# Kernel tuning notes

Hardware: AMD Instinct MI355X
Metric: run time of the kernel (lower is better)

The kernel has to match this reference:

```python
import jax, jax.numpy as jnp
import numpy as np

# Config constants (match init_kwargs)
N_EXPERTS = 8
CAPACITY = 1280
W_IMPORTANCE = 0.01
W_LOAD = 0.01
LAMBDA_Z = 0.001
W_PENALTY = 0.01


def setup_inputs() -> dict:
    key = jax.random.key(0)
    ks = jax.random.split(key, 6)
    B, T, C, E, F = 4, 2048, 1024, N_EXPERTS, 4096
    s = 0.02
    return {
        "x": jax.random.normal(ks[0], (B, T, C), dtype=jnp.float32),
        "gate_w": jax.random.normal(ks[1], (E, C), dtype=jnp.float32) * s,
        "gate_b": jnp.zeros((E,), dtype=jnp.float32),
        "w1": jax.random.normal(ks[2], (E, F, C), dtype=jnp.float32) * s,
        "b1": jnp.zeros((E, F), dtype=jnp.float32),
        "w2": jax.random.normal(ks[3], (E, C, F), dtype=jnp.float32) * s,
        "b2": jnp.zeros((E, C), dtype=jnp.float32),
    }


def reference(x, gate_w, gate_b, w1, b1, w2, b2):
    B, T, C = x.shape
    E = N_EXPERTS
    xf = x.reshape(B * T, C)
    bt = xf.shape[0]

    # ---- routing ----
    gate_logits = xf @ gate_w.T + gate_b  # (BT, E)

    # penalty loss
    p = jax.nn.softmax(gate_logits / 1.66, axis=-1)
    pen_a = jnp.mean(p * (1.0 - p))
    pm = p.mean(axis=0)
    pen_b = 1.0 / E - jnp.mean(pm * (1.0 - pm))
    penalty = W_PENALTY * (pen_a + pen_b)

    # z-loss
    z_loss = LAMBDA_Z * jnp.mean(jax.nn.logsumexp(gate_logits, axis=-1) ** 2)

    router_probs = jax.nn.softmax(gate_logits.astype(jnp.float32), axis=-1).astype(x.dtype)
    top1_idx = jnp.argmax(router_probs, axis=-1)        # (BT,)
    top1_w = jnp.max(router_probs, axis=-1)             # (BT,)
    onehot = jax.nn.one_hot(top1_idx, E, dtype=jnp.int32)

    # capacity masking: position of each token within its chosen expert
    priority = jnp.cumsum(onehot, axis=0)               # (BT, E)
    pos = priority[jnp.arange(bt), top1_idx] - 1        # (BT,)
    keep = pos < CAPACITY                               # (BT,) bool

    # load-balance loss
    f_i = onehot.astype(x.dtype).mean(axis=0)
    P_i = router_probs.mean(axis=0)
    load_loss = W_LOAD * E * jnp.sum(f_i * P_i)

    # importance loss (scatter of top1 probs == onehot-weighted sum)
    importance = (onehot.astype(x.dtype) * top1_w[:, None]).sum(axis=0)  # (E,)
    cv2 = jnp.var(importance) / jnp.mean(importance) ** 2
    importance_loss = W_IMPORTANCE * cv2

    aux_loss = penalty + z_loss + load_loss + importance_loss

    # ---- dispatch -> grouped FFN -> combine ----
    pos_c = jnp.clip(pos, 0, CAPACITY - 1)
    keep_f = keep.astype(x.dtype)[:, None]
    buf = jnp.zeros((E, CAPACITY, C), dtype=x.dtype).at[top1_idx, pos_c].add(xf * keep_f)
    h = jax.nn.gelu(jnp.einsum('ekc,efc->ekf', buf, w1) + b1[:, None, :], approximate=True)
    yb = jnp.einsum('ekf,ecf->ekc', h, w2) + b2[:, None, :]
    y = yb[top1_idx, pos_c] * keep_f                    # dropped tokens -> 0

    out = (top1_w[:, None] * y).reshape(B, T, C)
    return out, aux_loss
```

## Files before the change

### kernel.cpp

```cpp
#include <hip/hip_runtime.h>
#include <hip/hip_bf16.h>
#include <stdint.h>

#define BTOK 8192
#define CDIM 1024
#define NEXP 8
#define FDIM 4096
#define ECAP 1280

typedef __attribute__((ext_vector_type(8))) unsigned short u16x8;
typedef __attribute__((ext_vector_type(8))) __bf16 bf16x8;
typedef __attribute__((ext_vector_type(4))) float f32x4;

__device__ __forceinline__ unsigned short f2bf(float f) {
    unsigned int u = __builtin_bit_cast(unsigned int, f);
    u += 0x7FFFu + ((u >> 16) & 1u);
    return (unsigned short)(u >> 16);
}

__device__ __forceinline__ bf16x8 lds_load8(const unsigned short* p) {
    return __builtin_bit_cast(bf16x8, *(const u16x8*)p);
}

__device__ __forceinline__ float gelu_tanh(float v) {
    float u = 0.7978845608028654f * (v + 0.044715f * v * v * v);
    float e = __expf(2.0f * u);
    float t = 1.0f - 2.0f * __builtin_amdgcn_rcpf(e + 1.0f);
    return 0.5f * v * (1.0f + t);
}

__device__ __forceinline__ void glds16(const unsigned short* g, unsigned short* l) {
    __builtin_amdgcn_global_load_lds(
        (const __attribute__((address_space(1))) void*)g,
        (__attribute__((address_space(3))) void*)l,
        16, 0, 0);
}

__global__ __launch_bounds__(256) void cvt_kernel(
    const float* __restrict__ src, unsigned short* __restrict__ dst, int n8)
{
    int i = blockIdx.x * 256 + threadIdx.x;
    if (i >= n8) return;
    const float4* s = (const float4*)(src + (size_t)i * 8);
    float4 a = s[0], b = s[1];
    u16x8 o;
    o[0] = f2bf(a.x); o[1] = f2bf(a.y); o[2] = f2bf(a.z); o[3] = f2bf(a.w);
    o[4] = f2bf(b.x); o[5] = f2bf(b.y); o[6] = f2bf(b.z); o[7] = f2bf(b.w);
    *(u16x8*)(dst + (size_t)i * 8) = o;
}

__global__ __launch_bounds__(256) void gate_kernel(
    const float* __restrict__ x,
    const float* __restrict__ gw,
    const float* __restrict__ gb,
    float* __restrict__ logits)
{
    const int lane = threadIdx.x & 63;
    const int wave = threadIdx.x >> 6;
    const int tok = blockIdx.x * 4 + wave;
    const float* xr = x + (size_t)tok * CDIM + lane * 16;
    float xv[16];
#pragma unroll
    for (int j = 0; j < 4; j++) {
        float4 v = ((const float4*)xr)[j];
        xv[4 * j] = v.x; xv[4 * j + 1] = v.y; xv[4 * j + 2] = v.z; xv[4 * j + 3] = v.w;
    }
    float acc[8];
#pragma unroll
    for (int e = 0; e < 8; e++) {
        const float* wr = gw + e * CDIM + lane * 16;
        float s = 0.f;
#pragma unroll
        for (int j = 0; j < 4; j++) {
            float4 v = ((const float4*)wr)[j];
            s += xv[4 * j] * v.x + xv[4 * j + 1] * v.y + xv[4 * j + 2] * v.z + xv[4 * j + 3] * v.w;
        }
        acc[e] = s;
    }
#pragma unroll
    for (int e = 0; e < 8; e++) {
#pragma unroll
        for (int off = 32; off > 0; off >>= 1)
            acc[e] += __shfl_xor(acc[e], off);
    }
    if (lane == 0) {
#pragma unroll
        for (int e = 0; e < 8; e++)
            logits[(size_t)tok * 8 + e] = acc[e] + gb[e];
    }
}

__global__ __launch_bounds__(256) void route_kernel(
    const float* __restrict__ logits,
    int* __restrict__ top1i, float* __restrict__ top1w,
    int* __restrict__ toks, float* __restrict__ slotw,
    int* __restrict__ cnt, float* __restrict__ aux_out)
{
    const int tid = threadIdx.x;
    const int TPT = BTOK / 256;
    float psum[8] = {}, qsum[8] = {}, imp[8] = {};
    int cnte[8] = {};
    float pen_a_s = 0.f, z_s = 0.f;
    const float INV_T = 1.0f / 1.66f;

    for (int i = 0; i < TPT; i++) {
        int t = tid * TPT + i;
        float l[8];
#pragma unroll
        for (int e = 0; e < 8; e++) l[e] = logits[t * 8 + e];
        float m = l[0];
#pragma unroll
        for (int e = 1; e < 8; e++) m = fmaxf(m, l[e]);
        float ex[8], se = 0.f;
#pragma unroll
        for (int e = 0; e < 8; e++) { ex[e] = __expf(l[e] - m); se += ex[e]; }
        float inv = 1.0f / se;
#pragma unroll
        for (int e = 0; e < 8; e++) psum[e] += ex[e] * inv;
        int am = 0; float bl = l[0];
#pragma unroll
        for (int e = 1; e < 8; e++) if (l[e] > bl) { bl = l[e]; am = e; }
        float w = ex[am] * inv;
        imp[am] += w; cnte[am]++;
        top1i[t] = am; top1w[t] = w;
        float lse = m + __logf(se);
        z_s += lse * lse;
        float m2 = m * INV_T, se2 = 0.f, ex2[8];
#pragma unroll
        for (int e = 0; e < 8; e++) { ex2[e] = __expf(l[e] * INV_T - m2); se2 += ex2[e]; }
        float inv2 = 1.0f / se2;
#pragma unroll
        for (int e = 0; e < 8; e++) { float q = ex2[e] * inv2; pen_a_s += q * (1.f - q); qsum[e] += q; }
    }

    __shared__ int sc[256][8];
#pragma unroll
    for (int e = 0; e < 8; e++) sc[tid][e] = cnte[e];
    __syncthreads();
    for (int st = 1; st < 256; st <<= 1) {
        int v[8];
        bool act = (tid >= st);
        if (act) {
#pragma unroll
            for (int e = 0; e < 8; e++) v[e] = sc[tid - st][e];
        }
        __syncthreads();
        if (act) {
#pragma unroll
            for (int e = 0; e < 8; e++) sc[tid][e] += v[e];
        }
        __syncthreads();
    }
    int run[8], tot[8];
#pragma unroll
    for (int e = 0; e < 8; e++) {
        run[e] = (tid > 0) ? sc[tid - 1][e] : 0;
        tot[e] = sc[255][e];
    }
    for (int i = 0; i < TPT; i++) {
        int t = tid * TPT + i;
        int am = top1i[t];
        int pos = 0;
#pragma unroll
        for (int e = 0; e < 8; e++) if (e == am) pos = run[e]++;
        if (pos < ECAP) {
            toks[am * ECAP + pos] = t;
            slotw[am * ECAP + pos] = top1w[t];
        }
    }
    if (tid < 8) cnt[tid] = (tot[tid] < ECAP) ? tot[tid] : ECAP;

    __shared__ float red[26][256];
    red[0][tid] = pen_a_s;
    red[1][tid] = z_s;
#pragma unroll
    for (int e = 0; e < 8; e++) {
        red[2 + e][tid] = qsum[e];
        red[10 + e][tid] = psum[e];
        red[18 + e][tid] = imp[e];
    }
    __syncthreads();
    for (int st = 128; st > 0; st >>= 1) {
        if (tid < st) {
#pragma unroll
            for (int j = 0; j < 26; j++) red[j][tid] += red[j][tid + st];
        }
        __syncthreads();
    }
    if (tid == 0) {
        const float BTf = (float)BTOK;
        float pen_a = red[0][0] / (BTf * 8.f);
        float pb = 0.f;
        for (int e = 0; e < 8; e++) { float pm = red[2 + e][0] / BTf; pb += pm * (1.f - pm); }
        float pen_b = 0.125f - pb * 0.125f;
        float penalty = 0.01f * (pen_a + pen_b);
        float z = 0.001f * red[1][0] / BTf;
        float load = 0.f;
        for (int e = 0; e < 8; e++) load += ((float)tot[e] / BTf) * (red[10 + e][0] / BTf);
        load *= 0.01f * 8.f;
        float mu = 0.f;
        for (int e = 0; e < 8; e++) mu += red[18 + e][0];
        mu *= 0.125f;
        float var = 0.f;
        for (int e = 0; e < 8; e++) { float d = red[18 + e][0] - mu; var += d * d; }
        var *= 0.125f;
        float cv2 = var / (mu * mu);
        float aux = penalty + z + load + 0.01f * cv2;
        aux_out[0] = aux;
    }
}

__global__ __launch_bounds__(256) void ffn1_kernel(
    const unsigned short* __restrict__ xb,
    const unsigned short* __restrict__ w1b,
    const float* __restrict__ b1,
    const int* __restrict__ toks,
    const int* __restrict__ cnt,
    unsigned short* __restrict__ H)
{
    const int e = blockIdx.y;
    const int MT = ECAP / 128;
    const int nbq = (int)gridDim.x >> 3;
    const int bid = blockIdx.x;
    const int b2 = (bid & 7) * nbq + (bid >> 3);
    const int mt = b2 % MT;
    const int nt = b2 / MT;
    const int cnt_e = cnt[e];
    const int m0 = mt * 128;
    if (m0 >= cnt_e) return;
    const int n0 = nt * 128;
    const unsigned short* W = w1b + (size_t)e * FDIM * CDIM;
    const int* tk = toks + e * ECAP;

    __shared__ __align__(16) unsigned short As[128 * 64];
    __shared__ __align__(16) unsigned short Bs[128 * 64];

    const int tid = threadIdx.x;
    const int lane = tid & 63;
    const int wave = tid >> 6;
    const int wm = wave & 1;
    const int wn = wave >> 1;
    const int wbase = wave * 512;

    const unsigned short* gA[4];
    const unsigned short* gB[4];
#pragma unroll
    for (int j = 0; j < 4; j++) {
        int idx = j * 256 + tid;
        int r = idx >> 3;
        int ch = (idx & 7) ^ (r & 7);
        int row = m0 + r;
        int tokid = (row < cnt_e) ? tk[row] : 0;
        if ((unsigned)tokid >= BTOK) tokid = 0;
        gA[j] = xb + (size_t)tokid * CDIM + ch * 8;
        gB[j] = W + (size_t)(n0 + r) * CDIM + ch * 8;
    }
    f32x4 acc[4][4] = {};
    const int fr = lane & 15;
    const int kq = (lane >> 4) * 8;
    const int sw = (fr & 7) << 3;
    for (int k0 = 0; k0 < CDIM; k0 += 64) {
#pragma unroll
        for (int j = 0; j < 4; j++) {
            glds16(gA[j] + k0, As + j * 2048 + wbase);
            glds16(gB[j] + k0, Bs + j * 2048 + wbase);
        }
        __syncthreads();
#pragma unroll
        for (int kk = 0; kk < 64; kk += 32) {
            bf16x8 af[4], bfr[4];
#pragma unroll
            for (int i = 0; i < 4; i++) {
                af[i]  = lds_load8(&As[(wm * 64 + i * 16 + fr) * 64 + ((kk + kq) ^ sw)]);
                bfr[i] = lds_load8(&Bs[(wn * 64 + i * 16 + fr) * 64 + ((kk + kq) ^ sw)]);
            }
#pragma unroll
            for (int i = 0; i < 4; i++)
#pragma unroll
                for (int j = 0; j < 4; j++)
                    acc[i][j] = __builtin_amdgcn_mfma_f32_16x16x32_bf16(af[i], bfr[j], acc[i][j], 0, 0, 0);
        }
        __syncthreads();
    }
    const int cq = (lane >> 4) * 4;
#pragma unroll
    for (int i = 0; i < 4; i++) {
#pragma unroll
        for (int j = 0; j < 4; j++) {
            int n = n0 + wn * 64 + j * 16 + fr;
            float bias = b1[e * FDIM + n];
            size_t base = ((size_t)e * ECAP + (m0 + wm * 64 + i * 16 + cq)) * FDIM + n;
#pragma unroll
            for (int rr = 0; rr < 4; rr++) {
                float v = acc[i][j][rr] + bias;
                H[base + (size_t)rr * FDIM] = f2bf(gelu_tanh(v));
            }
        }
    }
}

__global__ __launch_bounds__(256) void ffn2_kernel(
    const unsigned short* __restrict__ H,
    const unsigned short* __restrict__ w2b,
    const float* __restrict__ b2,
    const int* __restrict__ toks,
    const float* __restrict__ slotw,
    const int* __restrict__ cnt,
    float* __restrict__ out)
{
    const int e = blockIdx.y;
    const int MT = ECAP / 128;
    const int nbq = (int)gridDim.x >> 3;
    const int bid = blockIdx.x;
    const int b2i = (bid & 7) * nbq + (bid >> 3);
    const int mt = b2i % MT;
    const int nt = b2i / MT;
    const int cnt_e = cnt[e];
    const int m0 = mt * 128;
    if (m0 >= cnt_e) return;
    const int n0 = nt * 128;
    const unsigned short* W = w2b + (size_t)e * CDIM * FDIM;
    const unsigned short* Hb = H + (size_t)e * ECAP * FDIM;

    __shared__ __align__(16) unsigned short As[128 * 64];
    __shared__ __align__(16) unsigned short Bs[128 * 64];

    const int tid = threadIdx.x;
    const int lane = tid & 63;
    const int wave = tid >> 6;
    const int wm = wave & 1;
    const int wn = wave >> 1;
    const int wbase = wave * 512;

    const unsigned short* gA[4];
    const unsigned short* gB[4];
#pragma unroll
    for (int j = 0; j < 4; j++) {
        int idx = j * 256 + tid;
        int r = idx >> 3;
        int ch = (idx & 7) ^ (r & 7);
        gA[j] = Hb + (size_t)(m0 + r) * FDIM + ch * 8;
        gB[j] = W + (size_t)(n0 + r) * FDIM + ch * 8;
    }
    f32x4 acc[4][4] = {};
    const int fr = lane & 15;
    const int kq = (lane >> 4) * 8;
    const int sw = (fr & 7) << 3;
    for (int k0 = 0; k0 < FDIM; k0 += 64) {
#pragma unroll
        for (int j = 0; j < 4; j++) {
            glds16(gA[j] + k0, As + j * 2048 + wbase);
            glds16(gB[j] + k0, Bs + j * 2048 + wbase);
        }
        __syncthreads();
#pragma unroll
        for (int kk = 0; kk < 64; kk += 32) {
            bf16x8 af[4], bfr[4];
#pragma unroll
            for (int i = 0; i < 4; i++) {
                af[i]  = lds_load8(&As[(wm * 64 + i * 16 + fr) * 64 + ((kk + kq) ^ sw)]);
                bfr[i] = lds_load8(&Bs[(wn * 64 + i * 16 + fr) * 64 + ((kk + kq) ^ sw)]);
            }
#pragma unroll
            for (int i = 0; i < 4; i++)
#pragma unroll
                for (int j = 0; j < 4; j++)
                    acc[i][j] = __builtin_amdgcn_mfma_f32_16x16x32_bf16(af[i], bfr[j], acc[i][j], 0, 0, 0);
        }
        __syncthreads();
    }
    const int cq = (lane >> 4) * 4;
#pragma unroll
    for (int i = 0; i < 4; i++) {
#pragma unroll
        for (int rr = 0; rr < 4; rr++) {
            int s = m0 + wm * 64 + i * 16 + cq + rr;
            if (s < cnt_e) {
                int t = toks[e * ECAP + s];
                float wgt = slotw[e * ECAP + s];
                if ((unsigned)t < BTOK) {
#pragma unroll
                    for (int j = 0; j < 4; j++) {
                        int n = n0 + wn * 64 + j * 16 + fr;
                        float y = acc[i][j][rr] + b2[e * CDIM + n];
                        out[(size_t)t * CDIM + n] = wgt * y;
                    }
                }
            }
        }
    }
}

extern "C" void kernel_launch(void* const* d_in, const int* in_sizes, int n_in,
                              void* d_out, int out_size, void* d_ws, size_t ws_size,
                              hipStream_t stream)
{
    (void)in_sizes; (void)n_in; (void)ws_size;
    const float* x  = (const float*)d_in[0];
    const float* gw = (const float*)d_in[1];
    const float* gb = (const float*)d_in[2];
    const float* w1 = (const float*)d_in[3];
    const float* b1 = (const float*)d_in[4];
    const float* w2 = (const float*)d_in[5];
    const float* b2 = (const float*)d_in[6];
    float* out = (float*)d_out;

    char* ws = (char*)d_ws;
    size_t off = 0;
    unsigned short* H   = (unsigned short*)(ws + off); off += (size_t)NEXP * ECAP * FDIM * 2;
    unsigned short* xb  = (unsigned short*)(ws + off); off += (size_t)BTOK * CDIM * 2;
    unsigned short* w1b = (unsigned short*)(ws + off); off += (size_t)NEXP * FDIM * CDIM * 2;
    unsigned short* w2b = (unsigned short*)(ws + off); off += (size_t)NEXP * CDIM * FDIM * 2;
    float* logits = (float*)(ws + off); off += (size_t)BTOK * 8 * 4;
    int* top1i    = (int*)(ws + off);   off += (size_t)BTOK * 4;
    float* top1w  = (float*)(ws + off); off += (size_t)BTOK * 4;
    int* toks     = (int*)(ws + off);   off += (size_t)NEXP * ECAP * 4;
    float* slotw  = (float*)(ws + off); off += (size_t)NEXP * ECAP * 4;
    int* cnt      = (int*)(ws + off);   off += (size_t)NEXP * 4;

    hipMemsetAsync(d_out, 0, (size_t)out_size * sizeof(float), stream);

    const int NX = BTOK * CDIM / 8;
    const int NW = NEXP * FDIM * CDIM / 8;
    cvt_kernel<<<(NX + 255) / 256, 256, 0, stream>>>(x, xb, NX);
    cvt_kernel<<<(NW + 255) / 256, 256, 0, stream>>>(w1, w1b, NW);
    cvt_kernel<<<(NW + 255) / 256, 256, 0, stream>>>(w2, w2b, NW);

    gate_kernel<<<BTOK / 4, 256, 0, stream>>>(x, gw, gb, logits);
    route_kernel<<<1, 256, 0, stream>>>(logits, top1i, top1w, toks, slotw, cnt,
                                        out + (size_t)BTOK * CDIM);
    ffn1_kernel<<<dim3((ECAP / 128) * (FDIM / 128), NEXP), 256, 0, stream>>>(xb, w1b, b1, toks, cnt, H);
    ffn2_kernel<<<dim3((ECAP / 128) * (CDIM / 128), NEXP), 256, 0, stream>>>(H, w2b, b2, toks, slotw, cnt, out);
}
```

Measured before the change: 711.9 us.

## Double-buffer LDS tiles in FFN GEMMs and fuse x bf16 conversion into gate

Both FFN GEMM kernels now use two LDS buffers, so the global-to-LDS load of the next K tile is issued before the MFMAs on the current tile, overlapping memory latency with compute. The separate x-to-bf16 conversion kernel is removed and the conversion is done inside the gate kernel, which already reads x, saving one pass over x and one launch. LDS use per block doubles to 64KB, which may lower occupancy.

```diff
diff --git a/kernel.cpp b/kernel.cpp
--- a/kernel.cpp
+++ b/kernel.cpp
@@ -34,6 +34,37 @@
         (const __attribute__((address_space(1))) void*)g,
         (__attribute__((address_space(3))) void*)l,
         16, 0, 0);
+}
+
+__device__ __forceinline__ void stage_tile(
+    const unsigned short* const* gA, const unsigned short* const* gB,
+    unsigned short* As, unsigned short* Bs, int wbase, int koff)
+{
+#pragma unroll
+    for (int j = 0; j < 4; j++) {
+        glds16(gA[j] + koff, As + j * 2048 + wbase);
+        glds16(gB[j] + koff, Bs + j * 2048 + wbase);
+    }
+}
+
+__device__ __forceinline__ void mfma_tile(
+    const unsigned short* As, const unsigned short* Bs,
+    int wm, int wn, int fr, int kq, int sw, f32x4 acc[4][4])
+{
+#pragma unroll
+    for (int kk = 0; kk < 64; kk += 32) {
+        bf16x8 af[4], bfr[4];
+#pragma unroll
+        for (int i = 0; i < 4; i++) {
+            af[i]  = lds_load8(&As[(wm * 64 + i * 16 + fr) * 64 + ((kk + kq) ^ sw)]);
+            bfr[i] = lds_load8(&Bs[(wn * 64 + i * 16 + fr) * 64 + ((kk + kq) ^ sw)]);
+        }
+#pragma unroll
+        for (int i = 0; i < 4; i++)
+#pragma unroll
+            for (int j = 0; j < 4; j++)
+                acc[i][j] = __builtin_amdgcn_mfma_f32_16x16x32_bf16(af[i], bfr[j], acc[i][j], 0, 0, 0);
+    }
 }
 
 __global__ __launch_bounds__(256) void cvt_kernel(
@@ -53,7 +84,8 @@
     const float* __restrict__ x,
     const float* __restrict__ gw,
     const float* __restrict__ gb,
-    float* __restrict__ logits)
+    float* __restrict__ logits,
+    unsigned short* __restrict__ xb)
 {
     const int lane = threadIdx.x & 63;
     const int wave = threadIdx.x >> 6;
@@ -65,6 +97,15 @@
         float4 v = ((const float4*)xr)[j];
         xv[4 * j] = v.x; xv[4 * j + 1] = v.y; xv[4 * j + 2] = v.z; xv[4 * j + 3] = v.w;
     }
+    u16x8 o0, o1;
+#pragma unroll
+    for (int j = 0; j < 8; j++) o0[j] = f2bf(xv[j]);
+#pragma unroll
+    for (int j = 0; j < 8; j++) o1[j] = f2bf(xv[8 + j]);
+    unsigned short* xo = xb + (size_t)tok * CDIM + lane * 16;
+    *(u16x8*)xo = o0;
+    *(u16x8*)(xo + 8) = o1;
+
     float acc[8];
 #pragma unroll
     for (int e = 0; e < 8; e++) {
@@ -232,8 +273,8 @@
     const unsigned short* W = w1b + (size_t)e * FDIM * CDIM;
     const int* tk = toks + e * ECAP;
 
-    __shared__ __align__(16) unsigned short As[128 * 64];
-    __shared__ __align__(16) unsigned short Bs[128 * 64];
+    __shared__ __align__(16) unsigned short As[2 * 128 * 64];
+    __shared__ __align__(16) unsigned short Bs[2 * 128 * 64];
 
     const int tid = threadIdx.x;
     const int lane = tid & 63;
@@ -259,27 +300,18 @@
     const int fr = lane & 15;
     const int kq = (lane >> 4) * 8;
     const int sw = (fr & 7) << 3;
-    for (int k0 = 0; k0 < CDIM; k0 += 64) {
-#pragma unroll
-        for (int j = 0; j < 4; j++) {
-            glds16(gA[j] + k0, As + j * 2048 + wbase);
-            glds16(gB[j] + k0, Bs + j * 2048 + wbase);
-        }
-        __syncthreads();
-#pragma unroll
-        for (int kk = 0; kk < 64; kk += 32) {
-            bf16x8 af[4], bfr[4];
-#pragma unroll
-            for (int i = 0; i < 4; i++) {
-                af[i]  = lds_load8(&As[(wm * 64 + i * 16 + fr) * 64 + ((kk + kq) ^ sw)]);
-                bfr[i] = lds_load8(&Bs[(wn * 64 + i * 16 + fr) * 64 + ((kk + kq) ^ sw)]);
-            }
-#pragma unroll
-            for (int i = 0; i < 4; i++)
-#pragma unroll
-                for (int j = 0; j < 4; j++)
-                    acc[i][j] = __builtin_amdgcn_mfma_f32_16x16x32_bf16(af[i], bfr[j], acc[i][j], 0, 0, 0);
-        }
+
+    stage_tile(gA, gB, As, Bs, wbase, 0);
+    __syncthreads();
+
+    const int NT = CDIM / 64;
+#pragma unroll 1
+    for (int t = 0; t < NT; t += 2) {
+        if (t + 1 < NT) stage_tile(gA, gB, As + 8192, Bs + 8192, wbase, (t + 1) * 64);
+        mfma_tile(As, Bs, wm, wn, fr, kq, sw, acc);
+        __syncthreads();
+        if (t + 2 < NT) stage_tile(gA, gB, As, Bs, wbase, (t + 2) * 64);
+        mfma_tile(As + 8192, Bs + 8192, wm, wn, fr, kq, sw, acc);
         __syncthreads();
     }
     const int cq = (lane >> 4) * 4;
@@ -322,8 +354,8 @@
     const unsigned short* W = w2b + (size_t)e * CDIM * FDIM;
     const unsigned short* Hb = H + (size_t)e * ECAP * FDIM;
 
-    __shared__ __align__(16) unsigned short As[128 * 64];
-    __shared__ __align__(16) unsigned short Bs[128 * 64];
+    __shared__ __align__(16) unsigned short As[2 * 128 * 64];
+    __shared__ __align__(16) unsigned short Bs[2 * 128 * 64];
 
     const int tid = threadIdx.x;
     const int lane = tid & 63;
@@ -346,27 +378,18 @@
     const int fr = lane & 15;
     const int kq = (lane >> 4) * 8;
     const int sw = (fr & 7) << 3;
-    for (int k0 = 0; k0 < FDIM; k0 += 64) {
-#pragma unroll
-        for (int j = 0; j < 4; j++) {
-            glds16(gA[j] + k0, As + j * 2048 + wbase);
-            glds16(gB[j] + k0, Bs + j * 2048 + wbase);
-        }
-        __syncthreads();
-#pragma unroll
-        for (int kk = 0; kk < 64; kk += 32) {
-            bf16x8 af[4], bfr[4];
-#pragma unroll
-            for (int i = 0; i < 4; i++) {
-                af[i]  = lds_load8(&As[(wm * 64 + i * 16 + fr) * 64 + ((kk + kq) ^ sw)]);
-                bfr[i] = lds_load8(&Bs[(wn * 64 + i * 16 + fr) * 64 + ((kk + kq) ^ sw)]);
-            }
-#pragma unroll
-            for (int i = 0; i < 4; i++)
-#pragma unroll
-                for (int j = 0; j < 4; j++)
-                    acc[i][j] = __builtin_amdgcn_mfma_f32_16x16x32_bf16(af[i], bfr[j], acc[i][j], 0, 0, 0);
-        }
+
+    stage_tile(gA, gB, As, Bs, wbase, 0);
+    __syncthreads();
+
+    const int NT = FDIM / 64;
+#pragma unroll 1
+    for (int t = 0; t < NT; t += 2) {
+        if (t + 1 < NT) stage_tile(gA, gB, As + 8192, Bs + 8192, wbase, (t + 1) * 64);
+        mfma_tile(As, Bs, wm, wn, fr, kq, sw, acc);
+        __syncthreads();
+        if (t + 2 < NT) stage_tile(gA, gB, As, Bs, wbase, (t + 2) * 64);
+        mfma_tile(As + 8192, Bs + 8192, wm, wn, fr, kq, sw, acc);
         __syncthreads();
     }
     const int cq = (lane >> 4) * 4;
@@ -420,13 +443,11 @@
 
     hipMemsetAsync(d_out, 0, (size_t)out_size * sizeof(float), stream);
 
-    const int NX = BTOK * CDIM / 8;
     const int NW = NEXP * FDIM * CDIM / 8;
-    cvt_kernel<<<(NX + 255) / 256, 256, 0, stream>>>(x, xb, NX);
     cvt_kernel<<<(NW + 255) / 256, 256, 0, stream>>>(w1, w1b, NW);
     cvt_kernel<<<(NW + 255) / 256, 256, 0, stream>>>(w2, w2b, NW);
 
-    gate_kernel<<<BTOK / 4, 256, 0, stream>>>(x, gw, gb, logits);
+    gate_kernel<<<BTOK / 4, 256, 0, stream>>>(x, gw, gb, logits, xb);
     route_kernel<<<1, 256, 0, stream>>>(logits, top1i, top1w, toks, slotw, cnt,
                                         out + (size_t)BTOK * CDIM);
     ffn1_kernel<<<dim3((ECAP / 128) * (FDIM / 128), NEXP), 256, 0, stream>>>(xb, w1b, b1, toks, cnt, H);
```

Result: no change. 698.2 us (-1.9%).
